# Optimization experiments

Hardware: AMD Instinct MI355X
Metric: run time of the kernel (lower is better)

The kernel has to match this reference:

```python
import jax, jax.numpy as jnp
import numpy as np

C, H, O, T, B = 15, 256, 512, 60, 1024


def setup_inputs() -> dict:
    key = jax.random.key(0)
    ks = jax.random.split(key, 8)
    s = 1.0 / np.sqrt(H)
    return {
        "x": jax.random.normal(ks[0], (B, H), dtype=jnp.float32),
        "cam": jax.random.randint(ks[1], (B,), 0, C, dtype=jnp.int32),
        "W_ih": jax.random.uniform(ks[2], (C, 3 * H, H), jnp.float32, -s, s),
        "W_hh": jax.random.uniform(ks[3], (C, 3 * H, H), jnp.float32, -s, s),
        "b_ih": jax.random.uniform(ks[4], (C, 3 * H), jnp.float32, -s, s),
        "b_hh": jax.random.uniform(ks[5], (C, 3 * H), jnp.float32, -s, s),
        "Wc": jax.random.uniform(ks[6], (C, O, H), jnp.float32, -s, s),
        "bc": jax.random.uniform(ks[7], (C, O), jnp.float32, -s, s),
    }


def reference(x, cam, W_ih, W_hh, b_ih, b_hh, Wc, bc):
    # Gather per-sample (per-camera) parameters once.
    Wi = W_ih[cam]          # [B, 3H, H]
    Wh = W_hh[cam]          # [B, 3H, H]
    bi = b_ih[cam]          # [B, 3H]
    bh = b_hh[cam]          # [B, 3H]
    Wcs = Wc[cam]           # [B, O, H]
    bcs = bc[cam]           # [B, O]

    # Input is constant across timesteps -> input gate preactivations computed once.
    gi = jnp.einsum('bh,bgh->bg', x, Wi) + bi   # [B, 3H]
    gi_r, gi_z, gi_n = jnp.split(gi, 3, axis=1)

    h0 = jnp.zeros_like(x)  # [B, H]

    def step(h, _):
        gh = jnp.einsum('bh,bgh->bg', h, Wh) + bh
        gh_r, gh_z, gh_n = jnp.split(gh, 3, axis=1)
        r = jax.nn.sigmoid(gi_r + gh_r)
        z = jax.nn.sigmoid(gi_z + gh_z)
        n = jnp.tanh(gi_n + r * gh_n)
        h_new = (1.0 - z) * n + z * h
        out = jax.nn.sigmoid(jnp.einsum('bh,boh->bo', h_new, Wcs) + bcs)  # [B, O]
        return h_new, out

    _, outs = jax.lax.scan(step, h0, None, length=T)  # [T, B, O]
    return jnp.transpose(outs, (1, 2, 0))             # [B, O, T]
```

## Files before the change

### kernel.cpp

```cpp
#include <hip/hip_runtime.h>
#include <hip/hip_fp16.h>

#define C_    15
#define H_    256
#define O_    512
#define T_    60
#define B_    1024
#define G3H_  768
#define TS    16
#define MAXG  12
#define NSLOT 96
#define NU    80
#define TCH   10

typedef __attribute__((ext_vector_type(8))) short bf16x8;
typedef __attribute__((ext_vector_type(4))) float f32x4;

__device__ __forceinline__ unsigned short f2bf(float f) {
    union { float f; unsigned u; } v; v.f = f;
    return (unsigned short)((v.u + 0x7FFFu + ((v.u >> 16) & 1u)) >> 16);
}
__device__ __forceinline__ float sigf(float x) { return 1.f / (1.f + __expf(-x)); }

__global__ __launch_bounds__(256) void sort_kernel(const int* __restrict__ cam,
    int* __restrict__ order, int* __restrict__ tcam, int* __restrict__ toff,
    int* __restrict__ tcnt)
{
    __shared__ int cnt[C_], start[C_], fill[C_];
    int tid = threadIdx.x;
    if (tid < C_) cnt[tid] = 0;
    if (tid < NSLOT) { tcam[tid] = -1; toff[tid] = 0; tcnt[tid] = 0; }
    __syncthreads();
    for (int b = tid; b < B_; b += 256) atomicAdd(&cnt[cam[b]], 1);
    __syncthreads();
    if (tid == 0) {
        int run = 0;
        for (int c = 0; c < C_; ++c) { start[c] = run; fill[c] = run; run += cnt[c]; }
    }
    __syncthreads();
    for (int b = tid; b < B_; b += 256) {
        int pos = atomicAdd(&fill[cam[b]], 1);
        order[pos] = b;
    }
    __syncthreads();
    if (tid == 0) {
        int gcnt[8] = {0,0,0,0,0,0,0,0};
        for (int c = 0; c < C_; ++c) gcnt[c & 7] += (cnt[c] + TS - 1) / TS;
        int maxg = 0;
        for (int g = 0; g < 8; ++g) maxg = max(maxg, gcnt[g]);
        if (maxg <= MAXG) {
            for (int g = 0; g < 8; ++g) {
                int k = 0;
                for (int c = g; c < C_; c += 8)
                    for (int r = 0; r < cnt[c]; r += TS) {
                        int slot = g + 8 * k;
                        tcam[slot] = c; toff[slot] = start[c] + r;
                        tcnt[slot] = min(TS, cnt[c] - r); ++k;
                    }
            }
        } else {
            int ti = 0;
            for (int c = 0; c < C_; ++c)
                for (int r = 0; r < cnt[c]; r += TS) {
                    tcam[ti] = c; toff[ti] = start[c] + r;
                    tcnt[ti] = min(TS, cnt[c] - r); ++ti;
                }
        }
    }
}

__global__ __launch_bounds__(256) void cvt_kernel(const float* __restrict__ src,
    unsigned short* __restrict__ dst, int n4)
{
    int i = blockIdx.x * 256 + threadIdx.x;
    if (i < n4) {
        float4 v = ((const float4*)src)[i];
        unsigned p0 = (unsigned)f2bf(v.x) | ((unsigned)f2bf(v.y) << 16);
        unsigned p1 = (unsigned)f2bf(v.z) | ((unsigned)f2bf(v.w) << 16);
        ((uint2*)dst)[i] = make_uint2(p0, p1);
    }
}

__global__ __launch_bounds__(64) void pack_kernel(
    const float* __restrict__ Whh, const float* __restrict__ Wc,
    unsigned short* __restrict__ Wpack)
{
    int cu = blockIdx.x;
    int c = cu / NU, u = cu - c * NU;
    int lane = threadIdx.x, q = lane >> 4, l16 = lane & 15;
    const float* src = (u < 48)
        ? &Whh[((size_t)c * G3H_ + u * 16 + l16) * H_]
        : &Wc[((size_t)c * O_ + (u - 48) * 16 + l16) * H_];
    unsigned short* dst = Wpack + ((size_t)cu * 8) * 512 + lane * 8;
#pragma unroll
    for (int kk = 0; kk < 8; ++kk) {
        float4 v0 = *(const float4*)&src[kk * 32 + q * 8];
        float4 v1 = *(const float4*)&src[kk * 32 + q * 8 + 4];
        unsigned short* d = dst + kk * 512;
        d[0] = f2bf(v0.x); d[1] = f2bf(v0.y); d[2] = f2bf(v0.z); d[3] = f2bf(v0.w);
        d[4] = f2bf(v1.x); d[5] = f2bf(v1.y); d[6] = f2bf(v1.z); d[7] = f2bf(v1.w);
    }
}

__global__ __launch_bounds__(384) void gi_mfma(
    const float* __restrict__ x, const unsigned short* __restrict__ Wih_b,
    const float* __restrict__ bih, const float* __restrict__ bhh,
    const int* __restrict__ order, const int* __restrict__ tcam,
    const int* __restrict__ toff, const int* __restrict__ tcnt,
    float* __restrict__ gi)
{
    int c = tcam[blockIdx.x]; if (c < 0) return;
    int cnt = tcnt[blockIdx.x], off = toff[blockIdx.x];
    int tid = threadIdx.x;
    __shared__ unsigned short hbfs[TS * 264];
    for (int idx = tid; idx < TS * 64; idx += 384) {
        int m = idx >> 6, c4 = idx & 63;
        float4 v = make_float4(0.f, 0.f, 0.f, 0.f);
        if (m < cnt) v = *(const float4*)&x[(size_t)order[off + m] * H_ + (c4 << 2)];
        unsigned p0 = (unsigned)f2bf(v.x) | ((unsigned)f2bf(v.y) << 16);
        unsigned p1 = (unsigned)f2bf(v.z) | ((unsigned)f2bf(v.w) << 16);
        *(uint2*)&hbfs[m * 264 + (c4 << 2)] = make_uint2(p0, p1);
    }
    __syncthreads();
    int w = tid >> 6, lane = tid & 63, q = lane >> 4, l16 = lane & 15;
    f32x4 acc[2][4];
#pragma unroll
    for (int i = 0; i < 2; ++i)
#pragma unroll
        for (int nt = 0; nt < 4; ++nt) acc[i][nt] = (f32x4){0.f, 0.f, 0.f, 0.f};
    const unsigned short* bp[2];
#pragma unroll
    for (int i = 0; i < 2; ++i)
        bp[i] = Wih_b + ((size_t)c * G3H_ + (2 * w + i) * 64 + l16) * H_;
    const unsigned short* ap = &hbfs[l16 * 264 + q * 8];
#pragma unroll 2
    for (int kk = 0; kk < 8; ++kk) {
        bf16x8 a = *(const bf16x8*)(ap + kk * 32);
#pragma unroll
        for (int i = 0; i < 2; ++i)
#pragma unroll
            for (int nt = 0; nt < 4; ++nt) {
                bf16x8 b = *(const bf16x8*)(bp[i] + (size_t)nt * 16 * H_ + kk * 32 + q * 8);
                acc[i][nt] = __builtin_amdgcn_mfma_f32_16x16x32_bf16(a, b, acc[i][nt], 0, 0, 0);
            }
    }
#pragma unroll
    for (int i = 0; i < 2; ++i) {
        int u = 2 * w + i;
#pragma unroll
        for (int nt = 0; nt < 4; ++nt) {
            int col = u * 64 + nt * 16 + l16;
            float bias = bih[c * G3H_ + col] + (col < 2 * H_ ? bhh[c * G3H_ + col] : 0.f);
#pragma unroll
            for (int r = 0; r < 4; ++r) {
                int m = q * 4 + r;
                gi[((size_t)(blockIdx.x * TS + m)) * G3H_ + col] = acc[i][nt][r] + bias;
            }
        }
    }
}

__global__ __launch_bounds__(512, 2) void persist_kernel(
    const unsigned short* __restrict__ Wpack, const float* __restrict__ bhh,
    const float* __restrict__ gi, const int* __restrict__ tcam,
    unsigned short* __restrict__ htraj)
{
    int slot = blockIdx.x;
    int c = tcam[slot]; if (c < 0) return;
    int tid = threadIdx.x, w = tid >> 6, lane = tid & 63, q = lane >> 4, l16 = lane & 15;

    __shared__ float gisT[G3H_][20];
    __shared__ unsigned short hbf[2][16][264];

    for (int idx = tid; idx < TS * G3H_; idx += 512) {
        int m = idx / G3H_, col = idx - m * G3H_;
        gisT[col][m] = gi[((size_t)(slot * TS + m)) * G3H_ + col];
    }

    bf16x8 wf[6][8];
#pragma unroll
    for (int ii = 0; ii < 3; ++ii)
#pragma unroll
        for (int jj = 0; jj < 2; ++jj)
#pragma unroll
            for (int kk = 0; kk < 8; ++kk)
                wf[ii * 2 + jj][kk] = *(const bf16x8*)(
                    Wpack + (((size_t)(c * NU + ii * 16 + w + 8 * jj)) * 8 + kk) * 512 + lane * 8);

    float bhn[2], hreg[2][4];
#pragma unroll
    for (int i = 0; i < 2; ++i) {
        int col = (w + 8 * i) * 16 + l16;
        bhn[i] = bhh[c * G3H_ + 2 * H_ + col];
#pragma unroll
        for (int r = 0; r < 4; ++r) hreg[i][r] = 0.f;
    }
    unsigned short* hp = htraj + ((size_t)slot * TS + q * 4) * 256 + w * 16 + l16;
    __syncthreads();

#pragma unroll 2
    for (int s = 0; s < T_; ++s) {
        int wbuf = s & 1, rbuf = wbuf ^ 1;
        f32x4 acc[6];
#pragma unroll
        for (int ui = 0; ui < 6; ++ui) acc[ui] = (f32x4){0.f, 0.f, 0.f, 0.f};
        if (s > 0) {
#pragma unroll
            for (int kk = 0; kk < 8; ++kk) {
                bf16x8 a = *(const bf16x8*)&hbf[rbuf][l16][kk * 32 + q * 8];
#pragma unroll
                for (int ui = 0; ui < 6; ++ui)
                    acc[ui] = __builtin_amdgcn_mfma_f32_16x16x32_bf16(a, wf[ui][kk], acc[ui], 0, 0, 0);
            }
        }
#pragma unroll
        for (int i = 0; i < 2; ++i) {
            int col = (w + 8 * i) * 16 + l16;
            f32x4 gr = *(const f32x4*)&gisT[col][q * 4];
            f32x4 gz = *(const f32x4*)&gisT[H_ + col][q * 4];
            f32x4 gn = *(const f32x4*)&gisT[2 * H_ + col][q * 4];
#pragma unroll
            for (int r = 0; r < 4; ++r) {
                float rr = sigf(gr[r] + acc[i][r]);
                float zz = sigf(gz[r] + acc[2 + i][r]);
                float pre = gn[r] + rr * (acc[4 + i][r] + bhn[i]);
                float nn = 2.f * sigf(2.f * pre) - 1.f;
                float hn = (1.f - zz) * nn + zz * hreg[i][r];
                hreg[i][r] = hn;
                unsigned short hb = f2bf(hn);
                hbf[wbuf][q * 4 + r][col] = hb;
                hp[r * 256 + i * 128] = hb;
            }
        }
        hp += (size_t)NSLOT * TS * 256;
        __syncthreads();
    }
}

__global__ __launch_bounds__(512, 2) void out_kernel(
    const unsigned short* __restrict__ Wpack, const float* __restrict__ bc,
    const unsigned short* __restrict__ htraj, const int* __restrict__ order,
    const int* __restrict__ tcam, const int* __restrict__ toff,
    const int* __restrict__ tcnt, unsigned short* __restrict__ outT,
    int direct, float* __restrict__ outp)
{
    int slot = blockIdx.x;
    int c = tcam[slot]; if (c < 0) return;
    int n = tcnt[slot], off = toff[slot];
    int tid = threadIdx.x, w = tid >> 6, lane = tid & 63, q = lane >> 4, l16 = lane & 15;
    __shared__ unsigned short hb[16][264];
    __shared__ int ord16[16];
    if (tid < 16) ord16[tid] = (tid < n) ? order[off + tid] : -1;

    bf16x8 wf[4][8];
    const unsigned short* wb = Wpack + ((size_t)c * NU + 48 + w * 4) * 8 * 512 + lane * 8;
#pragma unroll
    for (int ui = 0; ui < 4; ++ui)
#pragma unroll
        for (int kk = 0; kk < 8; ++kk)
            wf[ui][kk] = *(const bf16x8*)(wb + ((size_t)ui * 8 + kk) * 512);
    float bcr[4];
#pragma unroll
    for (int ui = 0; ui < 4; ++ui)
        bcr[ui] = bc[c * O_ + (w * 4 + ui) * 16 + l16];
    __syncthreads();

    for (int ti = 0; ti < TCH; ++ti) {
        int t = blockIdx.y * TCH + ti;
        {
            int m = tid >> 5, c8 = (tid & 31) * 8;
            uint4 v = *(const uint4*)&htraj[(((size_t)t * NSLOT + slot) * 16 + m) * 256 + c8];
            *(uint4*)&hb[m][c8] = v;
        }
        __syncthreads();
        f32x4 acc[4];
#pragma unroll
        for (int ui = 0; ui < 4; ++ui) acc[ui] = (f32x4){0.f, 0.f, 0.f, 0.f};
#pragma unroll
        for (int kk = 0; kk < 8; ++kk) {
            bf16x8 a = *(const bf16x8*)&hb[l16][kk * 32 + q * 8];
#pragma unroll
            for (int ui = 0; ui < 4; ++ui)
                acc[ui] = __builtin_amdgcn_mfma_f32_16x16x32_bf16(a, wf[ui][kk], acc[ui], 0, 0, 0);
        }
#pragma unroll
        for (int ui = 0; ui < 4; ++ui) {
            int o = (w * 4 + ui) * 16 + l16;
#pragma unroll
            for (int r = 0; r < 4; ++r) {
                int b = ord16[q * 4 + r];
                if (b >= 0) {
                    float val = sigf(acc[ui][r] + bcr[ui]);
                    if (direct) outp[((size_t)b * O_ + o) * T_ + t] = val;
                    else outT[((size_t)t * B_ + b) * O_ + o] =
                             __half_as_ushort(__float2half_rn(val));
                }
            }
        }
        __syncthreads();
    }
}

__global__ __launch_bounds__(256) void transpose_kernel(
    const unsigned short* __restrict__ outT, float* __restrict__ outp)
{
    int b = blockIdx.x, o0 = blockIdx.y * 64;
    __shared__ float ts[T_][65];
    int tid = threadIdx.x;
    for (int idx = tid; idx < T_ * 64; idx += 256) {
        int t = idx >> 6, o = idx & 63;
        ts[t][o] = __half2float(__ushort_as_half(outT[((size_t)t * B_ + b) * O_ + o0 + o]));
    }
    __syncthreads();
    for (int idx = tid; idx < 64 * T_; idx += 256) {
        int o = idx / T_, t = idx - o * T_;
        outp[((size_t)b * O_ + o0 + o) * T_ + t] = ts[t][o];
    }
}

extern "C" void kernel_launch(void* const* d_in, const int* in_sizes, int n_in,
                              void* d_out, int out_size, void* d_ws, size_t ws_size,
                              hipStream_t stream)
{
    const float* x   = (const float*)d_in[0];
    const int*   cam = (const int*)d_in[1];
    const float* Wih = (const float*)d_in[2];
    const float* Whh = (const float*)d_in[3];
    const float* bih = (const float*)d_in[4];
    const float* bhh = (const float*)d_in[5];
    const float* Wc  = (const float*)d_in[6];
    const float* bc  = (const float*)d_in[7];
    float* outp = (float*)d_out;

    char* w = (char*)d_ws;
    unsigned short* Wih_b = (unsigned short*)w; w += (size_t)C_ * G3H_ * H_ * 2;
    unsigned short* Wpack = (unsigned short*)w; w += (size_t)C_ * NU * 8 * 512 * 2;
    int* order = (int*)w; w += B_ * 4;
    int* tcam  = (int*)w; w += NSLOT * 4;
    int* toff  = (int*)w; w += NSLOT * 4;
    int* tcnt  = (int*)w; w += NSLOT * 4;
    float* gi  = (float*)w; w += (size_t)NSLOT * TS * G3H_ * 4;
    unsigned short* htraj = (unsigned short*)w; w += (size_t)T_ * NSLOT * 16 * 256 * 2;
    unsigned short* outT = (unsigned short*)w;
    size_t need = (size_t)(w - (char*)d_ws) + (size_t)T_ * B_ * O_ * 2;
    int direct = (ws_size < need) ? 1 : 0;

    sort_kernel<<<1, 256, 0, stream>>>(cam, order, tcam, toff, tcnt);
    cvt_kernel<<<(C_ * G3H_ * H_ / 4 + 255) / 256, 256, 0, stream>>>(Wih, Wih_b, C_ * G3H_ * H_ / 4);
    pack_kernel<<<C_ * NU, 64, 0, stream>>>(Whh, Wc, Wpack);
    gi_mfma<<<NSLOT, 384, 0, stream>>>(x, Wih_b, bih, bhh, order, tcam, toff, tcnt, gi);
    persist_kernel<<<NSLOT, 512, 0, stream>>>(Wpack, bhh, gi, tcam, htraj);
    out_kernel<<<dim3(NSLOT, T_ / TCH), 512, 0, stream>>>(Wpack, bc, htraj, order, tcam,
                                                          toff, tcnt, outT, direct, outp);
    if (!direct)
        transpose_kernel<<<dim3(B_, O_ / 64), 256, 0, stream>>>(outT, outp);
}
```

Measured before the change: 449.2 us.

## Fuse output projection into persistent GRU kernel with 1024-thread blocks

Merges the recurrent step and the per-timestep output projection into a single persistent kernel. Each block now runs 16 waves, and each wave holds gate and output weight fragments in registers, so the output MFMAs for step t-1 are issued alongside the gate MFMAs for step t. This removes the h-trajectory round trip through global memory and one kernel launch. In exchange, the output work and its scattered stores now sit on the serial recurrence critical path, and only 96 blocks do all of it, where the separate output kernel used 6x as many.

```diff
diff --git a/kernel.cpp b/kernel.cpp
--- a/kernel.cpp
+++ b/kernel.cpp
@@ -11,7 +11,6 @@
 #define MAXG  12
 #define NSLOT 96
 #define NU    80
-#define TCH   10
 
 typedef __attribute__((ext_vector_type(8))) short bf16x8;
 typedef __attribute__((ext_vector_type(4))) float f32x4;
@@ -160,144 +159,121 @@
     }
 }
 
-__global__ __launch_bounds__(512, 2) void persist_kernel(
+__global__ __launch_bounds__(1024, 1) void persist_kernel(
     const unsigned short* __restrict__ Wpack, const float* __restrict__ bhh,
-    const float* __restrict__ gi, const int* __restrict__ tcam,
-    unsigned short* __restrict__ htraj)
-{
-    int slot = blockIdx.x;
-    int c = tcam[slot]; if (c < 0) return;
-    int tid = threadIdx.x, w = tid >> 6, lane = tid & 63, q = lane >> 4, l16 = lane & 15;
-
-    __shared__ float gisT[G3H_][20];
-    __shared__ unsigned short hbf[2][16][264];
-
-    for (int idx = tid; idx < TS * G3H_; idx += 512) {
-        int m = idx / G3H_, col = idx - m * G3H_;
-        gisT[col][m] = gi[((size_t)(slot * TS + m)) * G3H_ + col];
-    }
-
-    bf16x8 wf[6][8];
-#pragma unroll
-    for (int ii = 0; ii < 3; ++ii)
-#pragma unroll
-        for (int jj = 0; jj < 2; ++jj)
-#pragma unroll
-            for (int kk = 0; kk < 8; ++kk)
-                wf[ii * 2 + jj][kk] = *(const bf16x8*)(
-                    Wpack + (((size_t)(c * NU + ii * 16 + w + 8 * jj)) * 8 + kk) * 512 + lane * 8);
-
-    float bhn[2], hreg[2][4];
-#pragma unroll
-    for (int i = 0; i < 2; ++i) {
-        int col = (w + 8 * i) * 16 + l16;
-        bhn[i] = bhh[c * G3H_ + 2 * H_ + col];
-#pragma unroll
-        for (int r = 0; r < 4; ++r) hreg[i][r] = 0.f;
-    }
-    unsigned short* hp = htraj + ((size_t)slot * TS + q * 4) * 256 + w * 16 + l16;
-    __syncthreads();
-
-#pragma unroll 2
-    for (int s = 0; s < T_; ++s) {
-        int wbuf = s & 1, rbuf = wbuf ^ 1;
-        f32x4 acc[6];
-#pragma unroll
-        for (int ui = 0; ui < 6; ++ui) acc[ui] = (f32x4){0.f, 0.f, 0.f, 0.f};
-        if (s > 0) {
-#pragma unroll
-            for (int kk = 0; kk < 8; ++kk) {
-                bf16x8 a = *(const bf16x8*)&hbf[rbuf][l16][kk * 32 + q * 8];
-#pragma unroll
-                for (int ui = 0; ui < 6; ++ui)
-                    acc[ui] = __builtin_amdgcn_mfma_f32_16x16x32_bf16(a, wf[ui][kk], acc[ui], 0, 0, 0);
-            }
-        }
-#pragma unroll
-        for (int i = 0; i < 2; ++i) {
-            int col = (w + 8 * i) * 16 + l16;
-            f32x4 gr = *(const f32x4*)&gisT[col][q * 4];
-            f32x4 gz = *(const f32x4*)&gisT[H_ + col][q * 4];
-            f32x4 gn = *(const f32x4*)&gisT[2 * H_ + col][q * 4];
-#pragma unroll
-            for (int r = 0; r < 4; ++r) {
-                float rr = sigf(gr[r] + acc[i][r]);
-                float zz = sigf(gz[r] + acc[2 + i][r]);
-                float pre = gn[r] + rr * (acc[4 + i][r] + bhn[i]);
-                float nn = 2.f * sigf(2.f * pre) - 1.f;
-                float hn = (1.f - zz) * nn + zz * hreg[i][r];
-                hreg[i][r] = hn;
-                unsigned short hb = f2bf(hn);
-                hbf[wbuf][q * 4 + r][col] = hb;
-                hp[r * 256 + i * 128] = hb;
-            }
-        }
-        hp += (size_t)NSLOT * TS * 256;
-        __syncthreads();
-    }
-}
-
-__global__ __launch_bounds__(512, 2) void out_kernel(
-    const unsigned short* __restrict__ Wpack, const float* __restrict__ bc,
-    const unsigned short* __restrict__ htraj, const int* __restrict__ order,
-    const int* __restrict__ tcam, const int* __restrict__ toff,
-    const int* __restrict__ tcnt, unsigned short* __restrict__ outT,
-    int direct, float* __restrict__ outp)
+    const float* __restrict__ bc, const float* __restrict__ gi,
+    const int* __restrict__ order, const int* __restrict__ tcam,
+    const int* __restrict__ toff, const int* __restrict__ tcnt,
+    unsigned short* __restrict__ outT, int direct, float* __restrict__ outp)
 {
     int slot = blockIdx.x;
     int c = tcam[slot]; if (c < 0) return;
     int n = tcnt[slot], off = toff[slot];
     int tid = threadIdx.x, w = tid >> 6, lane = tid & 63, q = lane >> 4, l16 = lane & 15;
-    __shared__ unsigned short hb[16][264];
-    __shared__ int ord16[16];
-    if (tid < 16) ord16[tid] = (tid < n) ? order[off + tid] : -1;
-
-    bf16x8 wf[4][8];
-    const unsigned short* wb = Wpack + ((size_t)c * NU + 48 + w * 4) * 8 * 512 + lane * 8;
-#pragma unroll
-    for (int ui = 0; ui < 4; ++ui)
+
+    __shared__ unsigned short hbf[2][16][264];
+
+    bf16x8 wg[3][8], wo[2][8];
+#pragma unroll
+    for (int ii = 0; ii < 3; ++ii)
 #pragma unroll
         for (int kk = 0; kk < 8; ++kk)
-            wf[ui][kk] = *(const bf16x8*)(wb + ((size_t)ui * 8 + kk) * 512);
-    float bcr[4];
-#pragma unroll
-    for (int ui = 0; ui < 4; ++ui)
-        bcr[ui] = bc[c * O_ + (w * 4 + ui) * 16 + l16];
-    __syncthreads();
-
-    for (int ti = 0; ti < TCH; ++ti) {
-        int t = blockIdx.y * TCH + ti;
-        {
-            int m = tid >> 5, c8 = (tid & 31) * 8;
-            uint4 v = *(const uint4*)&htraj[(((size_t)t * NSLOT + slot) * 16 + m) * 256 + c8];
-            *(uint4*)&hb[m][c8] = v;
-        }
-        __syncthreads();
-        f32x4 acc[4];
-#pragma unroll
-        for (int ui = 0; ui < 4; ++ui) acc[ui] = (f32x4){0.f, 0.f, 0.f, 0.f};
+            wg[ii][kk] = *(const bf16x8*)(
+                Wpack + (((size_t)(c * NU + ii * 16 + w)) * 8 + kk) * 512 + lane * 8);
+#pragma unroll
+    for (int ii = 0; ii < 2; ++ii)
+#pragma unroll
+        for (int kk = 0; kk < 8; ++kk)
+            wo[ii][kk] = *(const bf16x8*)(
+                Wpack + (((size_t)(c * NU + 48 + ii * 16 + w)) * 8 + kk) * 512 + lane * 8);
+
+    int col = w * 16 + l16;
+    float bhn = bhh[c * G3H_ + 2 * H_ + col];
+    float bcr[2];
+#pragma unroll
+    for (int ii = 0; ii < 2; ++ii) bcr[ii] = bc[c * O_ + (ii * 16 + w) * 16 + l16];
+    int bidx[4];
+#pragma unroll
+    for (int r = 0; r < 4; ++r) bidx[r] = (q * 4 + r < n) ? order[off + q * 4 + r] : -1;
+
+    float gir[4], giz[4], gin[4];
+#pragma unroll
+    for (int r = 0; r < 4; ++r) {
+        size_t row = (size_t)(slot * TS + q * 4 + r) * G3H_;
+        gir[r] = gi[row + col];
+        giz[r] = gi[row + H_ + col];
+        gin[r] = gi[row + 2 * H_ + col];
+    }
+    float hreg[4] = {0.f, 0.f, 0.f, 0.f};
+
+    for (int s = 0; s < T_; ++s) {
+        int wbuf = s & 1, rbuf = wbuf ^ 1;
+        f32x4 accg0 = (f32x4){0.f,0.f,0.f,0.f}, accg1 = accg0, accg2 = accg0;
+        f32x4 acco0 = accg0, acco1 = accg0;
+        if (s > 0) {
+#pragma unroll
+            for (int kk = 0; kk < 8; ++kk) {
+                bf16x8 a = *(const bf16x8*)&hbf[rbuf][l16][kk * 32 + q * 8];
+                accg0 = __builtin_amdgcn_mfma_f32_16x16x32_bf16(a, wg[0][kk], accg0, 0, 0, 0);
+                accg1 = __builtin_amdgcn_mfma_f32_16x16x32_bf16(a, wg[1][kk], accg1, 0, 0, 0);
+                accg2 = __builtin_amdgcn_mfma_f32_16x16x32_bf16(a, wg[2][kk], accg2, 0, 0, 0);
+                acco0 = __builtin_amdgcn_mfma_f32_16x16x32_bf16(a, wo[0][kk], acco0, 0, 0, 0);
+                acco1 = __builtin_amdgcn_mfma_f32_16x16x32_bf16(a, wo[1][kk], acco1, 0, 0, 0);
+            }
+            int t = s - 1;
+#pragma unroll
+            for (int ii = 0; ii < 2; ++ii) {
+                int o = (ii * 16 + w) * 16 + l16;
+                const f32x4& ao = ii ? acco1 : acco0;
+#pragma unroll
+                for (int r = 0; r < 4; ++r) {
+                    if (bidx[r] >= 0) {
+                        float val = sigf(ao[r] + bcr[ii]);
+                        if (direct) outp[((size_t)bidx[r] * O_ + o) * T_ + t] = val;
+                        else outT[((size_t)t * B_ + bidx[r]) * O_ + o] =
+                                 __half_as_ushort(__float2half_rn(val));
+                    }
+                }
+            }
+        }
+#pragma unroll
+        for (int r = 0; r < 4; ++r) {
+            float rr = sigf(gir[r] + accg0[r]);
+            float zz = sigf(giz[r] + accg1[r]);
+            float pre = gin[r] + rr * (accg2[r] + bhn);
+            float nn = 2.f * sigf(2.f * pre) - 1.f;
+            float hn = (1.f - zz) * nn + zz * hreg[r];
+            hreg[r] = hn;
+            hbf[wbuf][q * 4 + r][col] = f2bf(hn);
+        }
+        asm volatile("s_waitcnt lgkmcnt(0)" ::: "memory");
+        __builtin_amdgcn_s_barrier();
+        __builtin_amdgcn_sched_barrier(0);
+    }
+    {
+        const int rb = (T_ - 1) & 1;
+        f32x4 acco0 = (f32x4){0.f,0.f,0.f,0.f}, acco1 = acco0;
 #pragma unroll
         for (int kk = 0; kk < 8; ++kk) {
-            bf16x8 a = *(const bf16x8*)&hb[l16][kk * 32 + q * 8];
-#pragma unroll
-            for (int ui = 0; ui < 4; ++ui)
-                acc[ui] = __builtin_amdgcn_mfma_f32_16x16x32_bf16(a, wf[ui][kk], acc[ui], 0, 0, 0);
-        }
-#pragma unroll
-        for (int ui = 0; ui < 4; ++ui) {
-            int o = (w * 4 + ui) * 16 + l16;
+            bf16x8 a = *(const bf16x8*)&hbf[rb][l16][kk * 32 + q * 8];
+            acco0 = __builtin_amdgcn_mfma_f32_16x16x32_bf16(a, wo[0][kk], acco0, 0, 0, 0);
+            acco1 = __builtin_amdgcn_mfma_f32_16x16x32_bf16(a, wo[1][kk], acco1, 0, 0, 0);
+        }
+        int t = T_ - 1;
+#pragma unroll
+        for (int ii = 0; ii < 2; ++ii) {
+            int o = (ii * 16 + w) * 16 + l16;
+            const f32x4& ao = ii ? acco1 : acco0;
 #pragma unroll
             for (int r = 0; r < 4; ++r) {
-                int b = ord16[q * 4 + r];
-                if (b >= 0) {
-                    float val = sigf(acc[ui][r] + bcr[ui]);
-                    if (direct) outp[((size_t)b * O_ + o) * T_ + t] = val;
-                    else outT[((size_t)t * B_ + b) * O_ + o] =
+                if (bidx[r] >= 0) {
+                    float val = sigf(ao[r] + bcr[ii]);
+                    if (direct) outp[((size_t)bidx[r] * O_ + o) * T_ + t] = val;
+                    else outT[((size_t)t * B_ + bidx[r]) * O_ + o] =
                              __half_as_ushort(__float2half_rn(val));
                 }
             }
         }
-        __syncthreads();
     }
 }
 
@@ -340,7 +316,6 @@
     int* toff  = (int*)w; w += NSLOT * 4;
     int* tcnt  = (int*)w; w += NSLOT * 4;
     float* gi  = (float*)w; w += (size_t)NSLOT * TS * G3H_ * 4;
-    unsigned short* htraj = (unsigned short*)w; w += (size_t)T_ * NSLOT * 16 * 256 * 2;
     unsigned short* outT = (unsigned short*)w;
     size_t need = (size_t)(w - (char*)d_ws) + (size_t)T_ * B_ * O_ * 2;
     int direct = (ws_size < need) ? 1 : 0;
@@ -349,9 +324,8 @@
     cvt_kernel<<<(C_ * G3H_ * H_ / 4 + 255) / 256, 256, 0, stream>>>(Wih, Wih_b, C_ * G3H_ * H_ / 4);
     pack_kernel<<<C_ * NU, 64, 0, stream>>>(Whh, Wc, Wpack);
     gi_mfma<<<NSLOT, 384, 0, stream>>>(x, Wih_b, bih, bhh, order, tcam, toff, tcnt, gi);
-    persist_kernel<<<NSLOT, 512, 0, stream>>>(Wpack, bhh, gi, tcam, htraj);
-    out_kernel<<<dim3(NSLOT, T_ / TCH), 512, 0, stream>>>(Wpack, bc, htraj, order, tcam,
-                                                          toff, tcnt, outT, direct, outp);
+    persist_kernel<<<NSLOT, 1024, 0, stream>>>(Wpack, bhh, bc, gi, order, tcam, toff, tcnt,
+                                               outT, direct, outp);
     if (!direct)
         transpose_kernel<<<dim3(B_, O_ / 64), 256, 0, stream>>>(outT, outp);
 }
```

After: 1.055 ms. 2.35x slower.
